# Kernel optimization log

Measured on AMD Instinct MI355X. Metric: run time of the kernel, lower is better.

## Reference

```python
import jax, jax.numpy as jnp
import numpy as np

B = 16384          # scenes (batch_size)
K = 16             # vehicles per scene (1 hero + 15 neighbors)
IN_LEN = 16        # in_length
OUT_LEN = 25       # out_length
ALL_LEN = 41       # all_length
T_H = IN_LEN - 1
ENC = 64           # encoder_size
N = B * K
NN = B * (K - 1)


def setup_inputs() -> dict:
    key = jax.random.key(0)
    ks = jax.random.split(key, 20)
    scene = jax.random.normal(ks[0], (N, 2, ALL_LEN), jnp.float32)
    idx = jnp.arange(N, dtype=jnp.int32)
    hero_index = idx[::K]                 # hero is first vehicle of each group
    nbr_index = idx[idx % K != 0]         # remaining K-1 vehicles, group-major
    w = lambda k, s: jax.random.normal(k, s, jnp.float32) * 0.1
    return {
        'scene': scene, 'hero_index': hero_index, 'nbr_index': nbr_index,
        'W_h1': w(ks[1], (2 * IN_LEN, 32)), 'b_h1': w(ks[2], (32,)),
        'W_h2': w(ks[3], (32, ENC)), 'b_h2': w(ks[4], (ENC,)),
        'W_f1': w(ks[5], (2 * OUT_LEN, 32)), 'b_f1': w(ks[6], (32,)),
        'W_f2': w(ks[7], (32, ENC)), 'b_f2': w(ks[8], (ENC,)),
        'W_dyn': w(ks[9], (ENC, 32)), 'b_dyn': w(ks[10], (32,)),
        'W_nbr': w(ks[11], (2 * IN_LEN, ENC)), 'b_nbr': w(ks[12], (ENC,)),
        'W_out': w(ks[13], (96, 128)), 'b_out': w(ks[14], (128,)),
        'W_op': w(ks[15], (128, 1)), 'b_op': w(ks[16], (1,)),
    }


def reference(scene, hero_index, nbr_index,
              W_h1, b_h1, W_h2, b_h2, W_f1, b_f1, W_f2, b_f2,
              W_dyn, b_dyn, W_nbr, b_nbr, W_out, b_out, W_op, b_op):
    lrelu = lambda x: jax.nn.leaky_relu(x, 0.1)
    # per-scene reference pose = hero position at t_h, broadcast to all vehicles
    ref = scene[hero_index, :, T_H][:, :, None]              # (B,2,1)
    scene = scene - jnp.repeat(ref, K, axis=0)               # (N,2,ALL_LEN)
    # per-scene, per-channel scale = max |history| over vehicles and time
    scale = jnp.abs(scene[:, :, :IN_LEN]).reshape(B, K, 2, IN_LEN).max(axis=(1, 3))  # (B,2)
    scene = scene / jnp.repeat(scale, K, axis=0)[:, :, None]
    hero = scene[hero_index]                                 # (B,2,ALL_LEN)
    nbrs = scene[nbr_index]                                  # (NN,2,ALL_LEN)
    hist = hero[:, :, :IN_LEN].transpose(0, 2, 1)            # (B,IN_LEN,2)
    fut = hero[:, :, IN_LEN:IN_LEN + OUT_LEN].transpose(0, 2, 1)  # (B,OUT_LEN,2)
    nb_hist = nbrs[:, :, :IN_LEN].transpose(0, 2, 1)         # (NN,IN_LEN,2)
    rel = jnp.repeat(hist, K - 1, axis=0) - nb_hist          # (NN,IN_LEN,2)
    hist_f = hist.reshape(B, 2 * IN_LEN)
    fut_f = fut.reshape(B, 2 * OUT_LEN)
    rel_f = rel.reshape(NN, 2 * IN_LEN)
    # hero history encoder (mlp_net) + dyn_emb
    hist_enc = lrelu(lrelu(hist_f @ W_h1 + b_h1) @ W_h2 + b_h2)
    hist_enc = lrelu(hist_enc @ W_dyn + b_dyn)
    # neighbor relative encoder + per-scene max pool + dyn_emb
    rela_enc = lrelu(rel_f @ W_nbr + b_nbr)                  # (NN,ENC)
    pooled = rela_enc.reshape(B, K - 1, ENC).max(axis=1)     # (B,ENC)
    pooled = lrelu(pooled @ W_dyn + b_dyn)
    # future encoder (mlp_net_fut) + dyn_emb
    fut_enc = lrelu(lrelu(fut_f @ W_f1 + b_f1) @ W_f2 + b_f2)
    fut_enc = lrelu(fut_enc @ W_dyn + b_dyn)
    enc = jnp.concatenate([hist_enc, pooled, fut_enc], axis=1)  # (B,96)
    feature_enc = lrelu(enc @ W_out + b_out)                 # (B,128)
    logit = jax.nn.sigmoid(feature_enc @ W_op + b_op)        # (B,1)
    return logit, feature_enc
```

## Files before the change

kernel.cpp:

```cpp
#include <hip/hip_runtime.h>
#include <math.h>

#define NB 16384

typedef short short8 __attribute__((ext_vector_type(8)));
typedef float f32x4 __attribute__((ext_vector_type(4)));

__device__ __forceinline__ float lrelu(float x){ return x > 0.f ? x : 0.1f*x; }

__device__ __forceinline__ unsigned short f2b(float f){
  unsigned u = __builtin_bit_cast(unsigned, f);
  u = (u + 0x7fffu + ((u >> 16) & 1u)) >> 16;
  return (unsigned short)u;
}

#define MFMA(a,b,c) __builtin_amdgcn_mfma_f32_16x16x32_bf16((a),(b),(c),0,0,0)

__device__ __forceinline__ short8 afrag(const unsigned short* tile, int stride_us, int kbase){
  const int l = threadIdx.x & 63;
  return *(const short8*)(tile + (size_t)(l & 15) * stride_us + kbase + ((l >> 4) * 8));
}

__device__ __forceinline__ short8 ldfrag(const unsigned short* __restrict__ frags, int slot, int idx){
  return *(const short8*)(frags + ((size_t)((slot * 8 + idx) * 64 + (threadIdx.x & 63)) * 8));
}

__global__ __launch_bounds__(64) void prep_frags(
    const float* __restrict__ W_h1, const float* __restrict__ W_f1,
    const float* __restrict__ W_h2, const float* __restrict__ W_f2,
    const float* __restrict__ W_dyn, const float* __restrict__ W_nbr,
    const float* __restrict__ W_out, unsigned short* __restrict__ frags)
{
  const int bid = blockIdx.x;
  const int slot = bid >> 3, w = bid & 7;
  const int l = threadIdx.x;
  const int n16 = l & 15, q = l >> 4;
  short8 r = {0,0,0,0,0,0,0,0};
  #pragma unroll
  for (int e = 0; e < 8; ++e){
    const int p = q * 8 + e;
    int i = -1, n = -1, ldn = 0;
    const float* W = nullptr;
    switch (slot){
      case 0:  W = W_nbr; ldn = 64;  n = (w & 3) * 16 + n16; i = 2*(p&15) + (p>>4); break;
      case 1:  W = W_h1;  ldn = 32;  n = (w & 1) * 16 + n16; i = 2*(p&15) + (p>>4); break;
      case 2:  W = W_f1;  ldn = 32;  n = (w & 1) * 16 + n16; i = (p < 25) ? 2*p   : -1; break;
      case 3:  W = W_f1;  ldn = 32;  n = (w & 1) * 16 + n16; i = (p < 25) ? 2*p+1 : -1; break;
      case 4:  W = W_dyn; ldn = 32;  n = (w & 1) * 16 + n16; i = p;      break;
      case 5:  W = W_dyn; ldn = 32;  n = (w & 1) * 16 + n16; i = 32 + p; break;
      case 6:  W = W_h2;  ldn = 64;  n = (w & 3) * 16 + n16; i = p; break;
      case 7:  W = W_f2;  ldn = 64;  n = (w & 3) * 16 + n16; i = p; break;
      case 8:  W = W_out; ldn = 128; n = w * 16 + n16;       i = p;      break;
      case 9:  W = W_out; ldn = 128; n = w * 16 + n16;       i = 32 + p; break;
      case 10: W = W_out; ldn = 128; n = w * 16 + n16;       i = 64 + p; break;
    }
    const float v = (W && i >= 0) ? W[i * ldn + n] : 0.f;
    r[e] = (short)f2b(v);
  }
  *(short8*)(frags + (size_t)(bid * 64 + l) * 8) = r;
}

__global__ __launch_bounds__(256) void highway_fused(
    const float* __restrict__ scene,
    const unsigned short* __restrict__ frags,
    const float* __restrict__ b_h1, const float* __restrict__ b_h2,
    const float* __restrict__ b_f1, const float* __restrict__ b_f2,
    const float* __restrict__ b_dyn, const float* __restrict__ b_nbr,
    const float* __restrict__ b_out, const float* __restrict__ W_op,
    const float* __restrict__ b_op,
    float* __restrict__ logit, float* __restrict__ feat)
{
  __shared__ __align__(16) unsigned short S[9408];
  __shared__ float red[4][8];
  unsigned short* An    = S;
  unsigned short* Ah    = S + 5184;
  unsigned short* Af    = S + 5824;
  unsigned short* As2h  = S;
  unsigned short* As2f  = S + 1152;
  unsigned short* Aenc  = S + 2304;
  unsigned short* As1h  = S + 6976;
  unsigned short* As1f  = S + 7616;
  unsigned short* Apool = S + 8256;

  const int tid = threadIdx.x;
  const int w = tid >> 6, l = tid & 63;
  const int col = l & 15;
  const int g0 = blockIdx.x * 8;

  {
    const int g = tid >> 5, s = tid & 31;
    const int c = s >> 4, t = s & 15;
    const float* sc = scene + (size_t)(g0 + g) * 1312;

    float v[16];
    #pragma unroll
    for (int k = 0; k < 16; ++k) v[k] = sc[k * 82 + c * 41 + t];
    const float vf0 = sc[c * 41 + 16 + t];
    const float vf1 = (t < 9) ? sc[c * 41 + 32 + t] : 0.f;

    const float ref = __shfl(v[0], (l & 32) | (c << 4) | 15, 64);

    float m = 0.f;
    #pragma unroll
    for (int k = 0; k < 16; ++k) m = fmaxf(m, fabsf(v[k] - ref));
    m = fmaxf(m, __shfl_xor(m, 1, 64));
    m = fmaxf(m, __shfl_xor(m, 2, 64));
    m = fmaxf(m, __shfl_xor(m, 4, 64));
    m = fmaxf(m, __shfl_xor(m, 8, 64));
    const float inv = 1.f / m;

    Ah[g * 40 + c * 16 + t] = f2b((v[0] - ref) * inv);
    #pragma unroll
    for (int j = 1; j < 16; ++j)
      An[((j - 1) >> 1) * 648 + (((j - 1) & 1) * 8 + g) * 40 + c * 16 + t]
        = f2b((v[0] - v[j]) * inv);
    Af[g * 72 + c * 32 + t] = f2b((vf0 - ref) * inv);
    Af[g * 72 + c * 32 + 16 + t] = (t < 9) ? f2b((vf1 - ref) * inv) : (unsigned short)0;
    An[7 * 648 + (8 + (tid >> 5)) * 40 + (tid & 31)] = 0;
  }
  __syncthreads();

  {
    const short8 wn = ldfrag(frags, 0, w);
    const float bn = b_nbr[w * 16 + col];
    f32x4 pm = {-1e30f, -1e30f, -1e30f, -1e30f};
    #pragma unroll
    for (int jp = 0; jp < 8; ++jp){
      const short8 a = afrag(An + jp * 648, 40, 0);
      f32x4 acc = {0.f, 0.f, 0.f, 0.f};
      acc = MFMA(a, wn, acc);
      if (jp < 7 || l < 32){
        #pragma unroll
        for (int r = 0; r < 4; ++r) pm[r] = fmaxf(pm[r], lrelu(acc[r] + bn));
      }
    }
    #pragma unroll
    for (int r = 0; r < 4; ++r) pm[r] = fmaxf(pm[r], __shfl_xor(pm[r], 32, 64));
    if (l < 32){
      #pragma unroll
      for (int r = 0; r < 4; ++r)
        Apool[((l >> 4) * 4 + r) * 72 + w * 16 + col] = f2b(pm[r]);
    }

    if (w < 2){
      const short8 a = afrag(Ah, 40, 0);
      f32x4 acc = {0.f, 0.f, 0.f, 0.f};
      acc = MFMA(a, ldfrag(frags, 1, w), acc);
      const float bb = b_h1[w * 16 + col];
      #pragma unroll
      for (int r = 0; r < 4; ++r)
        As1h[((l >> 4) * 4 + r) * 40 + w * 16 + col] = f2b(lrelu(acc[r] + bb));
    } else {
      const int ct = w - 2;
      const short8 a0 = afrag(Af, 72, 0);
      const short8 a1 = afrag(Af, 72, 32);
      f32x4 acc = {0.f, 0.f, 0.f, 0.f};
      acc = MFMA(a0, ldfrag(frags, 2, ct), acc);
      acc = MFMA(a1, ldfrag(frags, 3, ct), acc);
      const float bb = b_f1[ct * 16 + col];
      #pragma unroll
      for (int r = 0; r < 4; ++r)
        As1f[((l >> 4) * 4 + r) * 40 + ct * 16 + col] = f2b(lrelu(acc[r] + bb));
    }
  }
  __syncthreads();

  if (w < 2){
    const short8 a0 = afrag(Apool, 72, 0);
    const short8 a1 = afrag(Apool, 72, 32);
    f32x4 acc = {0.f, 0.f, 0.f, 0.f};
    acc = MFMA(a0, ldfrag(frags, 4, w), acc);
    acc = MFMA(a1, ldfrag(frags, 5, w), acc);
    const float bd = b_dyn[w * 16 + col];
    #pragma unroll
    for (int r = 0; r < 4; ++r)
      Aenc[((l >> 4) * 4 + r) * 104 + 32 + w * 16 + col] = f2b(lrelu(acc[r] + bd));
    const short8 a = afrag(As1h, 40, 0);
    f32x4 acc2 = {0.f, 0.f, 0.f, 0.f};
    acc2 = MFMA(a, ldfrag(frags, 6, w), acc2);
    const float bh = b_h2[w * 16 + col];
    #pragma unroll
    for (int r = 0; r < 4; ++r)
      As2h[((l >> 4) * 4 + r) * 72 + w * 16 + col] = f2b(lrelu(acc2[r] + bh));
  } else {
    const short8 a = afrag(As1h, 40, 0);
    f32x4 acc = {0.f, 0.f, 0.f, 0.f};
    acc = MFMA(a, ldfrag(frags, 6, w), acc);
    const float bh = b_h2[w * 16 + col];
    #pragma unroll
    for (int r = 0; r < 4; ++r)
      As2h[((l >> 4) * 4 + r) * 72 + w * 16 + col] = f2b(lrelu(acc[r] + bh));
    const short8 af_ = afrag(As1f, 40, 0);
    #pragma unroll
    for (int u = 0; u < 2; ++u){
      const int ct = (w - 2) * 2 + u;
      f32x4 acc2 = {0.f, 0.f, 0.f, 0.f};
      acc2 = MFMA(af_, ldfrag(frags, 7, ct), acc2);
      const float bf = b_f2[ct * 16 + col];
      #pragma unroll
      for (int r = 0; r < 4; ++r)
        As2f[((l >> 4) * 4 + r) * 72 + ct * 16 + col] = f2b(lrelu(acc2[r] + bf));
    }
  }
  __syncthreads();

  {
    const unsigned short* src = (w < 2) ? As2h : As2f;
    const int ct = w & 1;
    const int base = (w < 2) ? 0 : 64;
    const short8 a0 = afrag(src, 72, 0);
    const short8 a1 = afrag(src, 72, 32);
    f32x4 acc = {0.f, 0.f, 0.f, 0.f};
    acc = MFMA(a0, ldfrag(frags, 4, ct), acc);
    acc = MFMA(a1, ldfrag(frags, 5, ct), acc);
    const float bd = b_dyn[ct * 16 + col];
    #pragma unroll
    for (int r = 0; r < 4; ++r)
      Aenc[((l >> 4) * 4 + r) * 104 + base + ct * 16 + col] = f2b(lrelu(acc[r] + bd));
  }
  __syncthreads();

  {
    const short8 a0 = afrag(Aenc, 104, 0);
    const short8 a1 = afrag(Aenc, 104, 32);
    const short8 a2 = afrag(Aenc, 104, 64);
    float psum[4] = {0.f, 0.f, 0.f, 0.f};
    #pragma unroll
    for (int u = 0; u < 2; ++u){
      const int ct = 2 * w + u;
      f32x4 acc = {0.f, 0.f, 0.f, 0.f};
      acc = MFMA(a0, ldfrag(frags, 8, ct), acc);
      acc = MFMA(a1, ldfrag(frags, 9, ct), acc);
      acc = MFMA(a2, ldfrag(frags, 10, ct), acc);
      const float bb = b_out[ct * 16 + col];
      const float wop = W_op[ct * 16 + col];
      if (l < 32){
        #pragma unroll
        for (int r = 0; r < 4; ++r){
          const int gg = (l >> 4) * 4 + r;
          const float fe = lrelu(acc[r] + bb);
          __builtin_nontemporal_store(fe, &feat[(size_t)(g0 + gg) * 128 + ct * 16 + col]);
          psum[r] += fe * wop;
        }
      }
    }
    #pragma unroll
    for (int r = 0; r < 4; ++r){
      psum[r] += __shfl_xor(psum[r], 1, 64);
      psum[r] += __shfl_xor(psum[r], 2, 64);
      psum[r] += __shfl_xor(psum[r], 4, 64);
      psum[r] += __shfl_xor(psum[r], 8, 64);
    }
    if (col == 0 && l < 32){
      #pragma unroll
      for (int r = 0; r < 4; ++r) red[w][(l >> 4) * 4 + r] = psum[r];
    }
  }
  __syncthreads();

  if (tid < 8){
    const float sacc = b_op[0] + red[0][tid] + red[1][tid] + red[2][tid] + red[3][tid];
    logit[g0 + tid] = 1.f / (1.f + expf(-sacc));
  }
}

extern "C" void kernel_launch(void* const* d_in, const int* in_sizes, int n_in,
                              void* d_out, int out_size, void* d_ws, size_t ws_size,
                              hipStream_t stream)
{
  (void)in_sizes; (void)n_in; (void)out_size; (void)ws_size;
  const float* scene = (const float*)d_in[0];
  const float* W_h1  = (const float*)d_in[3];
  const float* b_h1  = (const float*)d_in[4];
  const float* W_h2  = (const float*)d_in[5];
  const float* b_h2  = (const float*)d_in[6];
  const float* W_f1  = (const float*)d_in[7];
  const float* b_f1  = (const float*)d_in[8];
  const float* W_f2  = (const float*)d_in[9];
  const float* b_f2  = (const float*)d_in[10];
  const float* W_dyn = (const float*)d_in[11];
  const float* b_dyn = (const float*)d_in[12];
  const float* W_nbr = (const float*)d_in[13];
  const float* b_nbr = (const float*)d_in[14];
  const float* W_out = (const float*)d_in[15];
  const float* b_out = (const float*)d_in[16];
  const float* W_op  = (const float*)d_in[17];
  const float* b_op  = (const float*)d_in[18];

  unsigned short* frags = (unsigned short*)d_ws;

  float* logit = (float*)d_out;
  float* feat  = logit + NB;

  prep_frags<<<88, 64, 0, stream>>>(W_h1, W_f1, W_h2, W_f2, W_dyn, W_nbr, W_out, frags);
  highway_fused<<<NB / 8, 256, 0, stream>>>(scene, frags,
      b_h1, b_h2, b_f1, b_f2, b_dyn, b_nbr, b_out, W_op, b_op, logit, feat);
}
```

Before: 29.78 us.

## Vectorize scene loads per vehicle row and compute neighbor encoding by linearity

Each thread now loads one vehicle's 16-step history row with 16-byte vector loads instead of strided scalar loads. Normalized positions are written with short8 LDS stores, and the per-scene ref and inverse scale are kept in shared memory for a separate future-trajectory pass. The neighbor relative encoding uses linearity, W·(hero−nbr) = W·hero − W·nbr, computing the hero MFMA once and subtracting each neighbor's. This trades an extra barrier and phase for more coalesced global loads and wider LDS writes, and the subtraction may change bf16 rounding.

```diff
diff --git a/kernel.cpp b/kernel.cpp
--- a/kernel.cpp
+++ b/kernel.cpp
@@ -71,6 +71,7 @@
     float* __restrict__ logit, float* __restrict__ feat)
 {
   __shared__ __align__(16) unsigned short S[9408];
+  __shared__ float2 ivs[16];
   __shared__ float red[4][8];
   unsigned short* An    = S;
   unsigned short* Ah    = S + 5184;
@@ -86,52 +87,75 @@
   const int w = tid >> 6, l = tid & 63;
   const int col = l & 15;
   const int g0 = blockIdx.x * 8;
-
-  {
-    const int g = tid >> 5, s = tid & 31;
-    const int c = s >> 4, t = s & 15;
-    const float* sc = scene + (size_t)(g0 + g) * 1312;
+  const float* sb = scene + (size_t)g0 * 1312;
+
+  {
+    const int g = tid >> 5, k = (tid >> 1) & 15, c = tid & 1;
+    const float* row = sb + g * 1312 + k * 82 + c * 41;
 
     float v[16];
     #pragma unroll
-    for (int k = 0; k < 16; ++k) v[k] = sc[k * 82 + c * 41 + t];
-    const float vf0 = sc[c * 41 + 16 + t];
-    const float vf1 = (t < 9) ? sc[c * 41 + 32 + t] : 0.f;
-
-    const float ref = __shfl(v[0], (l & 32) | (c << 4) | 15, 64);
+    for (int q = 0; q < 4; ++q)
+      __builtin_memcpy(&v[4 * q], row + 4 * q, 16);
+
+    const float ref = __shfl(v[15], (l & 32) | (l & 1), 64);
 
     float m = 0.f;
     #pragma unroll
-    for (int k = 0; k < 16; ++k) m = fmaxf(m, fabsf(v[k] - ref));
-    m = fmaxf(m, __shfl_xor(m, 1, 64));
+    for (int t = 0; t < 16; ++t) m = fmaxf(m, fabsf(v[t] - ref));
     m = fmaxf(m, __shfl_xor(m, 2, 64));
     m = fmaxf(m, __shfl_xor(m, 4, 64));
     m = fmaxf(m, __shfl_xor(m, 8, 64));
+    m = fmaxf(m, __shfl_xor(m, 16, 64));
     const float inv = 1.f / m;
 
-    Ah[g * 40 + c * 16 + t] = f2b((v[0] - ref) * inv);
-    #pragma unroll
-    for (int j = 1; j < 16; ++j)
-      An[((j - 1) >> 1) * 648 + (((j - 1) & 1) * 8 + g) * 40 + c * 16 + t]
-        = f2b((v[0] - v[j]) * inv);
-    Af[g * 72 + c * 32 + t] = f2b((vf0 - ref) * inv);
-    Af[g * 72 + c * 32 + 16 + t] = (t < 9) ? f2b((vf1 - ref) * inv) : (unsigned short)0;
-    An[7 * 648 + (8 + (tid >> 5)) * 40 + (tid & 31)] = 0;
+    short8 r0, r1;
+    #pragma unroll
+    for (int t = 0; t < 8; ++t){
+      r0[t] = (short)f2b((v[t]     - ref) * inv);
+      r1[t] = (short)f2b((v[t + 8] - ref) * inv);
+    }
+    if (k == 0){
+      *(short8*)(Ah + g * 40 + c * 16)           = r0;
+      *(short8*)(Ah + g * 40 + c * 16 + 8)       = r1;
+      *(short8*)(Ah + (8 + g) * 40 + c * 16)     = r0;
+      *(short8*)(Ah + (8 + g) * 40 + c * 16 + 8) = r1;
+      ivs[g * 2 + c] = make_float2(ref, inv);
+    } else {
+      unsigned short* dst = An + ((k - 1) >> 1) * 648
+                          + ((((k - 1) & 1) << 3) + g) * 40 + c * 16;
+      *(short8*)dst       = r0;
+      *(short8*)(dst + 8) = r1;
+    }
+    if (tid < 160) *(unsigned*)(An + 4856 + 2 * tid) = 0u;
+  }
+  __syncthreads();
+
+  {
+    const int g = tid >> 5, c = (tid >> 4) & 1, t = tid & 15;
+    const float2 ri = ivs[g * 2 + c];
+    const float* fr = sb + g * 1312 + c * 41 + 16;
+    const float vf0 = fr[t];
+    Af[g * 72 + c * 32 + t] = f2b((vf0 - ri.x) * ri.y);
+    unsigned short hi = 0;
+    if (t < 9) hi = f2b((fr[16 + t] - ri.x) * ri.y);
+    Af[g * 72 + c * 32 + 16 + t] = hi;
   }
   __syncthreads();
 
   {
     const short8 wn = ldfrag(frags, 0, w);
     const float bn = b_nbr[w * 16 + col];
+    const f32x4 zero = {0.f, 0.f, 0.f, 0.f};
+    const f32x4 H = MFMA(afrag(Ah, 40, 0), wn, zero);
     f32x4 pm = {-1e30f, -1e30f, -1e30f, -1e30f};
     #pragma unroll
     for (int jp = 0; jp < 8; ++jp){
-      const short8 a = afrag(An + jp * 648, 40, 0);
-      f32x4 acc = {0.f, 0.f, 0.f, 0.f};
-      acc = MFMA(a, wn, acc);
+      const f32x4 N = MFMA(afrag(An + jp * 648, 40, 0), wn, zero);
       if (jp < 7 || l < 32){
         #pragma unroll
-        for (int r = 0; r < 4; ++r) pm[r] = fmaxf(pm[r], lrelu(acc[r] + bn));
+        for (int r = 0; r < 4; ++r)
+          pm[r] = fmaxf(pm[r], lrelu(H[r] - N[r] + bn));
       }
     }
     #pragma unroll
@@ -143,20 +167,17 @@
     }
 
     if (w < 2){
-      const short8 a = afrag(Ah, 40, 0);
       f32x4 acc = {0.f, 0.f, 0.f, 0.f};
-      acc = MFMA(a, ldfrag(frags, 1, w), acc);
+      acc = MFMA(afrag(Ah, 40, 0), ldfrag(frags, 1, w), acc);
       const float bb = b_h1[w * 16 + col];
       #pragma unroll
       for (int r = 0; r < 4; ++r)
         As1h[((l >> 4) * 4 + r) * 40 + w * 16 + col] = f2b(lrelu(acc[r] + bb));
     } else {
       const int ct = w - 2;
-      const short8 a0 = afrag(Af, 72, 0);
-      const short8 a1 = afrag(Af, 72, 32);
       f32x4 acc = {0.f, 0.f, 0.f, 0.f};
-      acc = MFMA(a0, ldfrag(frags, 2, ct), acc);
-      acc = MFMA(a1, ldfrag(frags, 3, ct), acc);
+      acc = MFMA(afrag(Af, 72, 0),  ldfrag(frags, 2, ct), acc);
+      acc = MFMA(afrag(Af, 72, 32), ldfrag(frags, 3, ct), acc);
       const float bb = b_f1[ct * 16 + col];
       #pragma unroll
       for (int r = 0; r < 4; ++r)
@@ -166,26 +187,22 @@
   __syncthreads();
 
   if (w < 2){
-    const short8 a0 = afrag(Apool, 72, 0);
-    const short8 a1 = afrag(Apool, 72, 32);
     f32x4 acc = {0.f, 0.f, 0.f, 0.f};
-    acc = MFMA(a0, ldfrag(frags, 4, w), acc);
-    acc = MFMA(a1, ldfrag(frags, 5, w), acc);
+    acc = MFMA(afrag(Apool, 72, 0),  ldfrag(frags, 4, w), acc);
+    acc = MFMA(afrag(Apool, 72, 32), ldfrag(frags, 5, w), acc);
     const float bd = b_dyn[w * 16 + col];
     #pragma unroll
     for (int r = 0; r < 4; ++r)
       Aenc[((l >> 4) * 4 + r) * 104 + 32 + w * 16 + col] = f2b(lrelu(acc[r] + bd));
-    const short8 a = afrag(As1h, 40, 0);
     f32x4 acc2 = {0.f, 0.f, 0.f, 0.f};
-    acc2 = MFMA(a, ldfrag(frags, 6, w), acc2);
+    acc2 = MFMA(afrag(As1h, 40, 0), ldfrag(frags, 6, w), acc2);
     const float bh = b_h2[w * 16 + col];
     #pragma unroll
     for (int r = 0; r < 4; ++r)
       As2h[((l >> 4) * 4 + r) * 72 + w * 16 + col] = f2b(lrelu(acc2[r] + bh));
   } else {
-    const short8 a = afrag(As1h, 40, 0);
     f32x4 acc = {0.f, 0.f, 0.f, 0.f};
-    acc = MFMA(a, ldfrag(frags, 6, w), acc);
+    acc = MFMA(afrag(As1h, 40, 0), ldfrag(frags, 6, w), acc);
     const float bh = b_h2[w * 16 + col];
     #pragma unroll
     for (int r = 0; r < 4; ++r)
@@ -208,11 +225,9 @@
     const unsigned short* src = (w < 2) ? As2h : As2f;
     const int ct = w & 1;
     const int base = (w < 2) ? 0 : 64;
-    const short8 a0 = afrag(src, 72, 0);
-    const short8 a1 = afrag(src, 72, 32);
     f32x4 acc = {0.f, 0.f, 0.f, 0.f};
-    acc = MFMA(a0, ldfrag(frags, 4, ct), acc);
-    acc = MFMA(a1, ldfrag(frags, 5, ct), acc);
+    acc = MFMA(afrag(src, 72, 0),  ldfrag(frags, 4, ct), acc);
+    acc = MFMA(afrag(src, 72, 32), ldfrag(frags, 5, ct), acc);
     const float bd = b_dyn[ct * 16 + col];
     #pragma unroll
     for (int r = 0; r < 4; ++r)
```

New measurement: 32.56 us. 1.09x slower.
